# Optimization experiments

Measured on AMD Instinct MI355X. Metric: run time of the kernel, lower is better.

## Reference

```python
import jax, jax.numpy as jnp
import numpy as np

T, B, D = 4096, 128, 64
H1, H2, H3 = 20, 10, 1
L1, L2 = 20, 10


def setup_inputs() -> dict:
    key = jax.random.key(0)
    ks = iter(jax.random.split(key, 24))
    s = 0.1
    rn = lambda k, shape: (jax.random.normal(k, shape, jnp.float32) * s)
    return dict(
        x=jax.random.normal(next(ks), (T, B, D), jnp.float32),
        # stack 1: layer 0 (input D -> H1), then L1-1 layers (H1 -> H1)
        s1_wih0=rn(next(ks), (H1, D)), s1_whh0=rn(next(ks), (H1, H1)),
        s1_bih0=rn(next(ks), (H1,)), s1_bhh0=rn(next(ks), (H1,)),
        s1_wih=rn(next(ks), (L1 - 1, H1, H1)), s1_whh=rn(next(ks), (L1 - 1, H1, H1)),
        s1_bih=rn(next(ks), (L1 - 1, H1)), s1_bhh=rn(next(ks), (L1 - 1, H1)),
        # stack 2: layer 0 (H1 -> H2), then L2-1 layers (H2 -> H2)
        s2_wih0=rn(next(ks), (H2, H1)), s2_whh0=rn(next(ks), (H2, H2)),
        s2_bih0=rn(next(ks), (H2,)), s2_bhh0=rn(next(ks), (H2,)),
        s2_wih=rn(next(ks), (L2 - 1, H2, H2)), s2_whh=rn(next(ks), (L2 - 1, H2, H2)),
        s2_bih=rn(next(ks), (L2 - 1, H2)), s2_bhh=rn(next(ks), (L2 - 1, H2)),
        # output stack: single layer (H2 -> 1)
        s3_wih=rn(next(ks), (H3, H2)), s3_whh=rn(next(ks), (H3, H3)),
        s3_bih=rn(next(ks), (H3,)), s3_bhh=rn(next(ks), (H3,)),
    )


def _rnn_layer(x, wih, whh, bih, bhh):
    # x: (T, B, In). torch nn.RNN tanh cell: h_t = tanh(W_ih x_t + b_ih + W_hh h_{t-1} + b_hh)
    xw = jnp.einsum('tbi,hi->tbh', x, wih) + bih  # hoist input projection out of the scan
    h0 = jnp.zeros((x.shape[1], whh.shape[0]), x.dtype)
    def step(h, xt):
        h = jnp.tanh(xt + h @ whh.T + bhh)
        return h, h
    hT, ys = jax.lax.scan(step, h0, xw)
    return ys, hT  # (T,B,H), (B,H)


def _stack(x, wihs, whhs, bihs, bhhs):
    # scan over homogeneous layers; carry is the full sequence
    def layer(carry, p):
        wih, whh, bih, bhh = p
        y, hT = _rnn_layer(carry, wih, whh, bih, bhh)
        return y, hT
    y, hTs = jax.lax.scan(layer, x, (wihs, whhs, bihs, bhhs))
    return y, hTs


def reference(x,
              s1_wih0, s1_whh0, s1_bih0, s1_bhh0, s1_wih, s1_whh, s1_bih, s1_bhh,
              s2_wih0, s2_whh0, s2_bih0, s2_bhh0, s2_wih, s2_whh, s2_bih, s2_bhh,
              s3_wih, s3_whh, s3_bih, s3_bhh):
    y, _ = _rnn_layer(x, s1_wih0, s1_whh0, s1_bih0, s1_bhh0)
    y, _ = _stack(y, s1_wih, s1_whh, s1_bih, s1_bhh)
    y, _ = _rnn_layer(y, s2_wih0, s2_whh0, s2_bih0, s2_bhh0)
    y, _ = _stack(y, s2_wih, s2_whh, s2_bih, s2_bhh)
    y, hT = _rnn_layer(y, s3_wih, s3_whh, s3_bih, s3_bhh)
    return y, hT[None]  # out: (T,B,1), hide: (1,B,1)
```

## Files before the change

kernel.cpp:

```cpp
#include <hip/hip_runtime.h>

#define DEVI __device__ __forceinline__
typedef float f2 __attribute__((ext_vector_type(2)));
typedef unsigned u32x2 __attribute__((ext_vector_type(2)));

constexpr int T_ = 4096, B_ = 128;
constexpr int CH = 8, NCH = T_ / CH;
constexpr int NSTEP2 = 528;
constexpr int XROW = 68;

constexpr int Y1L = 2 * CH * 20;
constexpr int Y2L = 2 * CH * 12;

struct P {
  const float* x;
  const float* w1; const float* b1;
  const float* wih[31]; const float* whh[31];
  const float* bih[31]; const float* bhh[31];
  float* out;
};

DEVI float ftanh(float x) {
  float e = __builtin_amdgcn_exp2f(x * 2.8853900817779268f);
  return 1.0f - 2.0f * __builtin_amdgcn_rcpf(e + 1.0f);
}

DEVI f2 pfma(f2 a, f2 b, f2 c) { return __builtin_elementwise_fma(a, b, c); }

DEVI void acc20u(f2& a, const float* r128, const float* r64, const f2* w) {
  float4 v0 = ((const float4*)r128)[0];
  float4 v1 = ((const float4*)r128)[1];
  float2 v2 = *(const float2*)r64;
  union { float4 f; f2 h[2]; } u0, u1; u0.f = v0; u1.f = v1;
  f2 t; t.x = v2.x; t.y = v2.y;
  a = pfma(u0.h[0], w[0], a);
  a = pfma(u0.h[1], w[1], a);
  a = pfma(u1.h[0], w[2], a);
  a = pfma(u1.h[1], w[3], a);
  a = pfma(t, w[4], a);
}

DEVI void acc12u(f2& a, const float* r128, const float* r64, const f2* w) {
  float4 v0 = *(const float4*)r128;
  float2 v2 = *(const float2*)r64;
  union { float4 f; f2 h[2]; } u; u.f = v0;
  f2 t; t.x = v2.x; t.y = v2.y;
  a = pfma(u.h[0], w[0], a);
  a = pfma(u.h[1], w[1], a);
  a = pfma(t, w[2], a);
}

DEVI float dot10(const float* r, const f2* w) {
  float4 v0 = ((const float4*)r)[0];
  float4 v1 = ((const float4*)r)[1];
  float2 v2 = *(const float2*)(r + 8);
  union { float4 f; f2 h[2]; } u0, u1; u0.f = v0; u1.f = v1;
  f2 a0{0.f, 0.f}, a1{0.f, 0.f};
  a0 = pfma(u0.h[0], w[0], a0);
  a1 = pfma(u0.h[1], w[1], a1);
  a0 = pfma(u1.h[0], w[2], a0);
  a1 = pfma(u1.h[1], w[3], a1);
  f2 t; t.x = v2.x; t.y = v2.y;
  a0 = pfma(t, w[4], a0);
  f2 s = a0 + a1;
  return s.x + s.y;
}

DEVI float redsum(f2 a) {
  const float s = a.x + a.y;
  u32x2 r = __builtin_amdgcn_permlane32_swap(__float_as_uint(s),
                                             __float_as_uint(s), false, false);
  return __uint_as_float(r.x) + __uint_as_float(r.y);
}

template <int SL>
DEVI void proj_chunk(const float* xbh, float* xww, const f2* wp, float bp,
                     bool hi) {
#pragma unroll
  for (int tt = 0; tt < CH; tt++) {
    const float* xr = xbh + SL * (CH * XROW) + tt * XROW;
    f2 a; a.x = bp; a.y = 0.f;
#pragma unroll
    for (int q = 0; q < 8; q++) {
      float4 v = ((const float4*)xr)[q];
      union { float4 f; f2 h[2]; } u; u.f = v;
      a = pfma(u.h[0], wp[2 * q], a);
      a = pfma(u.h[1], wp[2 * q + 1], a);
    }
    const float s = redsum(a);
    if (!hi) xww[SL * (CH * 20) + tt * 20] = s;
  }
}

template <int SL>
DEVI void l30_chunk(const float* y29, const f2* wi30, float b30, float wh30,
                    float& h30, float*& optr, bool st) {
#pragma unroll
  for (int tt = 0; tt < CH; tt++) {
    const float d = dot10(y29 + SL * (CH * 12) + tt * 12, wi30);
    h30 = ftanh(fmaf(h30, wh30, d + b30));
    if (st) optr[tt * B_] = h30;
  }
  optr += CH * B_;
}

DEVI void stage_proj(const P& p, int b, int lane, float* xb, float* xwf,
                     const float* y29) {
  const int jj = lane & 31;
  const bool act = jj < 20;
  const bool hi = lane >= 32;
  const int j = act ? jj : 19;
  const int ko = hi ? 32 : 0;
  f2 wp[16];
#pragma unroll
  for (int k = 0; k < 16; k++) {
    wp[k].x = p.w1[j * 64 + ko + 2 * k]; wp[k].y = p.w1[j * 64 + ko + 2 * k + 1];
  }
  const float bp = hi ? 0.f : p.b1[j];
  float* xww = xwf + j;
  const float* xbh = xb + ko;

  f2 wi30[5];
#pragma unroll
  for (int k = 0; k < 5; k++) {
    wi30[k].x = p.wih[30][2 * k];
    wi30[k].y = p.wih[30][2 * k + 1];
  }
  const float b30 = p.bih[30][0] + p.bhh[30][0];
  const float wh30 = p.whh[30][0];
  float h30 = 0.f;
  float* optr = p.out + b;
  const bool st = (lane == 0);

  const int tq = lane >> 4, qq = lane & 15;
  const float* src[2]; int dst[2];
#pragma unroll
  for (int r = 0; r < 2; r++) {
    const int row = r * 4 + tq;
    src[r] = p.x + (size_t)row * (B_ * 64) + (size_t)b * 64 + qq * 4;
    dst[r] = row * XROW + qq * 4;
  }
  float4 pf[2];
#pragma unroll
  for (int r = 0; r < 2; r++) pf[r] = *(const float4*)src[r];
#pragma unroll
  for (int r = 0; r < 2; r++) *(float4*)(xb + dst[r]) = pf[r];
#pragma unroll
  for (int r = 0; r < 2; r++) src[r] += CH * B_ * 64;

  for (int s = 0; s < NSTEP2; s += 2) {
    {
      const int c = s;
      if (c < NCH) {
        const bool more = (c + 1 < NCH);
        float4 nx[2];
        if (more) {
#pragma unroll
          for (int r = 0; r < 2; r++) { nx[r] = *(const float4*)src[r]; src[r] += CH * B_ * 64; }
        }
        if (act) proj_chunk<0>(xbh, xww, wp, bp, hi);
        if (more) {
#pragma unroll
          for (int r = 0; r < 2; r++) *(float4*)(xb + CH * XROW + dst[r]) = nx[r];
        }
      }
      if ((unsigned)(s - 16) < (unsigned)NCH)
        l30_chunk<0>(y29, wi30, b30, wh30, h30, optr, st);
      __syncthreads();
    }
    {
      const int c = s + 1;
      if (c < NCH) {
        const bool more = (c + 1 < NCH);
        float4 nx[2];
        if (more) {
#pragma unroll
          for (int r = 0; r < 2; r++) { nx[r] = *(const float4*)src[r]; src[r] += CH * B_ * 64; }
        }
        if (act) proj_chunk<1>(xbh, xww, wp, bp, hi);
        if (more) {
#pragma unroll
          for (int r = 0; r < 2; r++) *(float4*)(xb + dst[r]) = nx[r];
        }
      }
      if ((unsigned)(s + 1 - 16) < (unsigned)NCH)
        l30_chunk<1>(y29, wi30, b30, wh30, h30, optr, st);
      __syncthreads();
    }
  }
  if (st) p.out[T_ * B_ + b] = h30;
}

template <int SL, bool FIRST>
DEVI void pair_chunk(const float* yin, const float* yinB,
                     const float* yArA, const float* yArB, float* yAw,
                     const float* yBrA, const float* yBrB, float* yBw,
                     const f2* wiA, const f2* whA, const f2* wiB, const f2* whB,
                     float bA, float bB, bool hi) {
  constexpr int BASE = SL * (CH * 20);
  constexpr int PV0  = (1 - SL) * (CH * 20) + (CH - 1) * 20;
  {
    f2 a; a.x = bA; a.y = 0.f;
    if constexpr (FIRST) { const float pick = yin[BASE]; if (!hi) a.x += pick; }
    else acc20u(a, yin + BASE, yinB + BASE, wiA);
    acc20u(a, yArA + PV0, yArB + PV0, whA);
    yAw[BASE] = ftanh(redsum(a));
  }
#pragma unroll
  for (int tt = 1; tt < CH; tt++) {
    const int IN  = BASE + tt * 20;
    const int INp = IN - 20;
    const int PVB = (tt == 1) ? PV0 : (INp - 20);
    f2 bb; bb.x = bB; bb.y = 0.f;
    acc20u(bb, yArA + INp, yArB + INp, wiB);
    acc20u(bb, yBrA + PVB, yBrB + PVB, whB);
    f2 a; a.x = bA; a.y = 0.f;
    if constexpr (FIRST) { const float pick = yin[IN]; if (!hi) a.x += pick; }
    else acc20u(a, yin + IN, yinB + IN, wiA);
    acc20u(a, yArA + INp, yArB + INp, whA);
    yBw[INp] = ftanh(redsum(bb));
    yAw[IN] = ftanh(redsum(a));
  }
  {
    const int IN = BASE + (CH - 1) * 20;
    f2 bb; bb.x = bB; bb.y = 0.f;
    acc20u(bb, yArA + IN, yArB + IN, wiB);
    acc20u(bb, yBrA + IN - 20, yBrB + IN - 20, whB);
    yBw[IN] = ftanh(redsum(bb));
  }
}

template <bool PH, bool FIRST>
DEVI void pair_s1(int la, int w, const P& p, int lane, float* y1f, float* xwf) {
  const int jj = lane & 31;
  const bool act = jj < 20;
  const bool hi = lane >= 32;
  const int j = act ? jj : 19;
  const int o128 = hi ? 12 : 0, o64 = hi ? 10 : 8;
  const int lb = la + 1;
  f2 whA[5], whB[5], wiB[5], wiA[FIRST ? 1 : 5];
#pragma unroll
  for (int q = 0; q < 5; q++) {
    const int tb = hi ? (q < 4 ? 12 + 2 * q : 10) : 2 * q;
    whA[q].x = p.whh[la][j * 20 + tb]; whA[q].y = p.whh[la][j * 20 + tb + 1];
    whB[q].x = p.whh[lb][j * 20 + tb]; whB[q].y = p.whh[lb][j * 20 + tb + 1];
    wiB[q].x = p.wih[lb][j * 20 + tb]; wiB[q].y = p.wih[lb][j * 20 + tb + 1];
    if constexpr (!FIRST) {
      wiA[q].x = p.wih[la][j * 20 + tb]; wiA[q].y = p.wih[la][j * 20 + tb + 1];
    }
  }
  float bA = p.bhh[la][j];
  if constexpr (!FIRST) bA += p.bih[la][j];
  float bB = p.bih[lb][j] + p.bhh[lb][j];
  if (hi) { bA = 0.f; bB = 0.f; }

  const float* yin  = FIRST ? (xwf + j) : (y1f + (la - 1) * Y1L + o128);
  const float* yinB = FIRST ? nullptr   : (y1f + (la - 1) * Y1L + o64);
  const float* yArA = y1f + la * Y1L + o128;
  const float* yArB = y1f + la * Y1L + o64;
  float*       yAw  = y1f + la * Y1L + j;
  const float* yBrA = y1f + lb * Y1L + o128;
  const float* yBrB = y1f + lb * Y1L + o64;
  float*       yBw  = y1f + lb * Y1L + j;
  if (act) { yAw[(2 * CH - 1) * 20] = 0.f; yBw[(2 * CH - 1) * 20] = 0.f; }

  for (int s = 0; s < NSTEP2; s += 2) {
    if ((unsigned)(s - w) < (unsigned)NCH && act)
      pair_chunk<PH ? 1 : 0, FIRST>(yin, yinB, yArA, yArB, yAw, yBrA, yBrB, yBw,
                                    wiA, whA, wiB, whB, bA, bB, hi);
    __syncthreads();
    if ((unsigned)(s + 1 - w) < (unsigned)NCH && act)
      pair_chunk<PH ? 0 : 1, FIRST>(yin, yinB, yArA, yArB, yAw, yBrA, yBrB, yBw,
                                    wiA, whA, wiB, whB, bA, bB, hi);
    __syncthreads();
  }
}

template <int SL, bool WIDE>
DEVI void s2pair_chunk(const float* yi0A, const float* yi0B,
                       const float* rArA, const float* rArB, float* rAw,
                       const float* rBrA, const float* rBrB, float* rBw,
                       const f2* wiA, const f2* whA, const f2* wiB, const f2* whB,
                       float bA, float bB) {
  constexpr int B1  = SL * (CH * 20);
  constexpr int B2  = SL * (CH * 12);
  constexpr int PV0 = (1 - SL) * (CH * 12) + (CH - 1) * 12;
  {
    f2 a; a.x = bA; a.y = 0.f;
    if constexpr (WIDE) acc20u(a, yi0A + B1, yi0B + B1, wiA);
    else                acc12u(a, yi0A + B2, yi0B + B2, wiA);
    acc12u(a, rArA + PV0, rArB + PV0, whA);
    rAw[B2] = ftanh(redsum(a));
  }
#pragma unroll
  for (int tt = 1; tt < CH; tt++) {
    const int IN2 = B2 + tt * 12;
    const int INp = IN2 - 12;
    const int PVB = (tt == 1) ? PV0 : (INp - 12);
    f2 bb; bb.x = bB; bb.y = 0.f;
    acc12u(bb, rArA + INp, rArB + INp, wiB);
    acc12u(bb, rBrA + PVB, rBrB + PVB, whB);
    f2 a; a.x = bA; a.y = 0.f;
    if constexpr (WIDE) { const int IN1 = B1 + tt * 20; acc20u(a, yi0A + IN1, yi0B + IN1, wiA); }
    else                acc12u(a, yi0A + IN2, yi0B + IN2, wiA);
    acc12u(a, rArA + INp, rArB + INp, whA);
    rBw[INp] = ftanh(redsum(bb));
    rAw[IN2] = ftanh(redsum(a));
  }
  {
    const int IN2 = B2 + (CH - 1) * 12;
    f2 bb; bb.x = bB; bb.y = 0.f;
    acc12u(bb, rArA + IN2, rArB + IN2, wiB);
    acc12u(bb, rBrA + IN2 - 12, rBrB + IN2 - 12, whB);
    rBw[IN2] = ftanh(redsum(bb));
  }
}

template <bool PH, bool WIDE>
DEVI void s2pair(int lA, int w, int rin, const P& p, int lane,
                 float* y1f, float* y2f) {
  const int jj = lane & 31;
  const bool act = jj < 10;
  const bool hi = lane >= 32;
  const int j = act ? jj : 9;
  const int o128w = hi ? 12 : 0, o64w = hi ? 10 : 8;
  const int o128s = hi ? 8 : 0,  o64s = hi ? 6 : 4;
  const int lB = lA + 1;
  f2 wiA[WIDE ? 5 : 3], whA[3], wiB[3], whB[3];
  if constexpr (WIDE) {
#pragma unroll
    for (int q = 0; q < 5; q++) {
      const int tb = hi ? (q < 4 ? 12 + 2 * q : 10) : 2 * q;
      wiA[q].x = p.wih[lA][j * 20 + tb];
      wiA[q].y = p.wih[lA][j * 20 + tb + 1];
    }
  } else {
#pragma unroll
    for (int q = 0; q < 3; q++) {
      const int tb = hi ? (q == 0 ? 8 : q == 1 ? 10 : 6) : 2 * q;
      wiA[q].x = tb     < 10 ? p.wih[lA][j * 10 + tb]     : 0.f;
      wiA[q].y = tb + 1 < 10 ? p.wih[lA][j * 10 + tb + 1] : 0.f;
    }
  }
#pragma unroll
  for (int q = 0; q < 3; q++) {
    const int tb = hi ? (q == 0 ? 8 : q == 1 ? 10 : 6) : 2 * q;
    whA[q].x = tb     < 10 ? p.whh[lA][j * 10 + tb]     : 0.f;
    whA[q].y = tb + 1 < 10 ? p.whh[lA][j * 10 + tb + 1] : 0.f;
    wiB[q].x = tb     < 10 ? p.wih[lB][j * 10 + tb]     : 0.f;
    wiB[q].y = tb + 1 < 10 ? p.wih[lB][j * 10 + tb + 1] : 0.f;
    whB[q].x = tb     < 10 ? p.whh[lB][j * 10 + tb]     : 0.f;
    whB[q].y = tb + 1 < 10 ? p.whh[lB][j * 10 + tb + 1] : 0.f;
  }
  const float bA = hi ? 0.f : (p.bih[lA][j] + p.bhh[lA][j]);
  const float bB = hi ? 0.f : (p.bih[lB][j] + p.bhh[lB][j]);

  const int rA = lA - 20;
  const float* yi0A = WIDE ? (y1f + 19 * Y1L + o128w) : (y2f + rin * Y2L + o128s);
  const float* yi0B = WIDE ? (y1f + 19 * Y1L + o64w)  : (y2f + rin * Y2L + o64s);
  const float* rArA = y2f + rA * Y2L + o128s;
  const float* rArB = y2f + rA * Y2L + o64s;
  float*       rAw  = y2f + rA * Y2L + j;
  const float* rBrA = y2f + (rA + 1) * Y2L + o128s;
  const float* rBrB = y2f + (rA + 1) * Y2L + o64s;
  float*       rBw  = y2f + (rA + 1) * Y2L + j;

  if constexpr (WIDE) {
    for (int q = lane; q < 10 * Y2L; q += 64) y2f[q] = 0.f;
  }

  for (int s = 0; s < NSTEP2; s += 2) {
    if ((unsigned)(s - w) < (unsigned)NCH && act)
      s2pair_chunk<PH ? 1 : 0, WIDE>(yi0A, yi0B, rArA, rArB, rAw, rBrA, rBrB, rBw,
                                     wiA, whA, wiB, whB, bA, bB);
    __syncthreads();
    if ((unsigned)(s + 1 - w) < (unsigned)NCH && act)
      s2pair_chunk<PH ? 0 : 1, WIDE>(yi0A, yi0B, rArA, rArB, rAw, rBrA, rBrB, rBw,
                                     wiA, whA, wiB, whB, bA, bB);
    __syncthreads();
  }
}

__global__ __launch_bounds__(1024, 1) void rnn_fused(P p) {
  __shared__ alignas(16) float xbuf[2 * CH * XROW];
  __shared__ alignas(16) float xw[2 * CH * 20];
  __shared__ alignas(16) float y1[20 * Y1L];
  __shared__ alignas(16) float y2[10 * Y2L];
  const int w = threadIdx.x >> 6, lane = threadIdx.x & 63, b = blockIdx.x;
  if (w == 0)       stage_proj(p, b, lane, xbuf, xw, y2 + 9 * Y2L);
  else if (w == 1)  pair_s1<true, true>(0, 1, p, lane, y1, xw);
  else if (w <= 10) {
    const int la = 2 * (w - 1);
    if (w & 1) pair_s1<true, false>(la, w, p, lane, y1, xw);
    else       pair_s1<false, false>(la, w, p, lane, y1, xw);
  }
  else if (w == 11) s2pair<true,  true >(20, 11, 0, p, lane, y1, y2);
  else if (w == 12) s2pair<false, false>(22, 12, 1, p, lane, y1, y2);
  else if (w == 13) s2pair<true,  false>(24, 13, 3, p, lane, y1, y2);
  else if (w == 14) s2pair<false, false>(26, 14, 5, p, lane, y1, y2);
  else              s2pair<true,  false>(28, 15, 7, p, lane, y1, y2);
}

extern "C" void kernel_launch(void* const* d_in, const int* in_sizes, int n_in,
                              void* d_out, int out_size, void* d_ws, size_t ws_size,
                              hipStream_t stream) {
  (void)in_sizes; (void)out_size; (void)d_ws; (void)ws_size;
  if (n_in < 21) return;
  P p{};
  p.x  = (const float*)d_in[0];
  p.w1 = (const float*)d_in[1];
  p.b1 = (const float*)d_in[3];
  p.wih[0] = nullptr;              p.whh[0] = (const float*)d_in[2];
  p.bih[0] = nullptr;              p.bhh[0] = (const float*)d_in[4];
  for (int l = 1; l < 20; l++) {
    p.wih[l] = (const float*)d_in[5] + (l - 1) * 400;
    p.whh[l] = (const float*)d_in[6] + (l - 1) * 400;
    p.bih[l] = (const float*)d_in[7] + (l - 1) * 20;
    p.bhh[l] = (const float*)d_in[8] + (l - 1) * 20;
  }
  p.wih[20] = (const float*)d_in[9];   p.whh[20] = (const float*)d_in[10];
  p.bih[20] = (const float*)d_in[11];  p.bhh[20] = (const float*)d_in[12];
  for (int l = 21; l < 30; l++) {
    p.wih[l] = (const float*)d_in[13] + (l - 21) * 100;
    p.whh[l] = (const float*)d_in[14] + (l - 21) * 100;
    p.bih[l] = (const float*)d_in[15] + (l - 21) * 10;
    p.bhh[l] = (const float*)d_in[16] + (l - 21) * 10;
  }
  p.wih[30] = (const float*)d_in[17];  p.whh[30] = (const float*)d_in[18];
  p.bih[30] = (const float*)d_in[19];  p.bhh[30] = (const float*)d_in[20];
  p.out = (float*)d_out;

  rnn_fused<<<B_, 1024, 0, stream>>>(p);
}
```

Baseline: 1.607 ms.

## Split each batch's layer pipeline across two workgroups linked by a global ring

Each batch element's wavefront pipeline is now split across two 576-thread workgroups instead of one 1024-thread workgroup. The first block runs the input projection and layers 0-13. The second runs layers 14-30. Layer-13 output passes between them through a 16-chunk ring buffer in workspace memory, with producer and consumer counters held as agent-scope atomics and spin-wait sleeps. The aim is to spread the 31-layer wavefront over twice as many CUs and shorten per-block barrier chains. The cost is global-memory handoff latency, spin-waiting, and a reliance on both blocks of a pair being resident at the same time.

```diff
diff --git a/kernel.cpp b/kernel.cpp
--- a/kernel.cpp
+++ b/kernel.cpp
@@ -11,6 +11,10 @@
 
 constexpr int Y1L = 2 * CH * 20;
 constexpr int Y2L = 2 * CH * 12;
+
+constexpr int RQ = 16;
+constexpr int NSF = NCH + 8;
+constexpr int NSB = NCH + 20;
 
 struct P {
   const float* x;
@@ -191,12 +195,70 @@
   if (st) p.out[T_ * B_ + b] = h30;
 }
 
-template <int SL, bool FIRST>
+DEVI void stage_proj_f(const P& p, int b, int lane, float* xb, float* xwf,
+                       int nstep) {
+  const int jj = lane & 31;
+  const bool act = jj < 20;
+  const bool hi = lane >= 32;
+  const int j = act ? jj : 19;
+  const int ko = hi ? 32 : 0;
+  f2 wp[16];
+#pragma unroll
+  for (int k = 0; k < 16; k++) {
+    wp[k].x = p.w1[j * 64 + ko + 2 * k]; wp[k].y = p.w1[j * 64 + ko + 2 * k + 1];
+  }
+  const float bp = hi ? 0.f : p.b1[j];
+  float* xww = xwf + j;
+  const float* xbh = xb + ko;
+
+  const int tq = lane >> 4, qq = lane & 15;
+  const float* src[2]; int dst[2];
+#pragma unroll
+  for (int r = 0; r < 2; r++) {
+    const int row = r * 4 + tq;
+    src[r] = p.x + (size_t)row * (B_ * 64) + (size_t)b * 64 + qq * 4;
+    dst[r] = row * XROW + qq * 4;
+  }
+  float4 pf[2];
+#pragma unroll
+  for (int r = 0; r < 2; r++) pf[r] = *(const float4*)src[r];
+#pragma unroll
+  for (int r = 0; r < 2; r++) *(float4*)(xb + dst[r]) = pf[r];
+#pragma unroll
+  for (int r = 0; r < 2; r++) src[r] += CH * B_ * 64;
+
+  for (int s = 0; s < nstep; s += 2) {
+#pragma unroll
+    for (int ph = 0; ph < 2; ph++) {
+      const int c = s + ph;
+      if (c < NCH) {
+        const bool more = (c + 1 < NCH);
+        float4 nx[2];
+        if (more) {
+#pragma unroll
+          for (int r = 0; r < 2; r++) { nx[r] = *(const float4*)src[r]; src[r] += CH * B_ * 64; }
+        }
+        if (act) {
+          if (c & 1) proj_chunk<1>(xbh, xww, wp, bp, hi);
+          else       proj_chunk<0>(xbh, xww, wp, bp, hi);
+        }
+        if (more) {
+          const int sl = ((c + 1) & 1) * (CH * XROW);
+#pragma unroll
+          for (int r = 0; r < 2; r++) *(float4*)(xb + sl + dst[r]) = nx[r];
+        }
+      }
+      __syncthreads();
+    }
+  }
+}
+
+template <int SL, bool FIRST, bool PROD = false>
 DEVI void pair_chunk(const float* yin, const float* yinB,
                      const float* yArA, const float* yArB, float* yAw,
                      const float* yBrA, const float* yBrB, float* yBw,
                      const f2* wiA, const f2* whA, const f2* wiB, const f2* whB,
-                     float bA, float bB, bool hi) {
+                     float bA, float bB, bool hi, float* gw = nullptr) {
   constexpr int BASE = SL * (CH * 20);
   constexpr int PV0  = (1 - SL) * (CH * 20) + (CH - 1) * 20;
   {
@@ -218,7 +280,9 @@
     if constexpr (FIRST) { const float pick = yin[IN]; if (!hi) a.x += pick; }
     else acc20u(a, yin + IN, yinB + IN, wiA);
     acc20u(a, yArA + INp, yArB + INp, whA);
-    yBw[INp] = ftanh(redsum(bb));
+    const float hb = ftanh(redsum(bb));
+    yBw[INp] = hb;
+    if constexpr (PROD) { if (!hi) gw[(tt - 1) * 20] = hb; }
     yAw[IN] = ftanh(redsum(a));
   }
   {
@@ -226,7 +290,9 @@
     f2 bb; bb.x = bB; bb.y = 0.f;
     acc20u(bb, yArA + IN, yArB + IN, wiB);
     acc20u(bb, yBrA + IN - 20, yBrB + IN - 20, whB);
-    yBw[IN] = ftanh(redsum(bb));
+    const float hb = ftanh(redsum(bb));
+    yBw[IN] = hb;
+    if constexpr (PROD) { if (!hi) gw[(CH - 1) * 20] = hb; }
   }
 }
 
@@ -273,6 +339,71 @@
       pair_chunk<PH ? 0 : 1, FIRST>(yin, yinB, yArA, yArB, yAw, yBrA, yBrB, yBw,
                                     wiA, whA, wiB, whB, bA, bB, hi);
     __syncthreads();
+  }
+}
+
+template <bool FIRST, bool PROD>
+DEVI void pair_drv(int la, int w, int nstep, const P& p, int lane,
+                   const float* xwf, const float* rIn, float* rA, float* rB,
+                   float* gring, unsigned* prog, unsigned* cons) {
+  const int jj = lane & 31;
+  const bool act = jj < 20;
+  const bool hi = lane >= 32;
+  const int j = act ? jj : 19;
+  const int o128 = hi ? 12 : 0, o64 = hi ? 10 : 8;
+  const int lb = la + 1;
+  f2 whA[5], whB[5], wiB[5], wiA[FIRST ? 1 : 5];
+#pragma unroll
+  for (int q = 0; q < 5; q++) {
+    const int tb = hi ? (q < 4 ? 12 + 2 * q : 10) : 2 * q;
+    whA[q].x = p.whh[la][j * 20 + tb]; whA[q].y = p.whh[la][j * 20 + tb + 1];
+    whB[q].x = p.whh[lb][j * 20 + tb]; whB[q].y = p.whh[lb][j * 20 + tb + 1];
+    wiB[q].x = p.wih[lb][j * 20 + tb]; wiB[q].y = p.wih[lb][j * 20 + tb + 1];
+    if constexpr (!FIRST) {
+      wiA[q].x = p.wih[la][j * 20 + tb]; wiA[q].y = p.wih[la][j * 20 + tb + 1];
+    }
+  }
+  float bA = p.bhh[la][j];
+  if constexpr (!FIRST) bA += p.bih[la][j];
+  float bB = p.bih[lb][j] + p.bhh[lb][j];
+  if (hi) { bA = 0.f; bB = 0.f; }
+
+  const float* yin  = FIRST ? (xwf + j) : (rIn + o128);
+  const float* yinB = FIRST ? nullptr   : (rIn + o64);
+  const float* yArA = rA + o128; const float* yArB = rA + o64;
+  float* yAw = rA + j;
+  const float* yBrA = rB + o128; const float* yBrB = rB + o64;
+  float* yBw = rB + j;
+  if (act) { yAw[(2 * CH - 1) * 20] = 0.f; yBw[(2 * CH - 1) * 20] = 0.f; }
+
+  for (int s = 0; s < nstep; s += 2) {
+#pragma unroll
+    for (int ph = 0; ph < 2; ph++) {
+      const int c = s + ph - w;
+      if ((unsigned)c < (unsigned)NCH && act) {
+        float* gw = nullptr;
+        if constexpr (PROD) {
+          if (c >= RQ) {
+            while ((int)c - (int)__hip_atomic_load(cons, __ATOMIC_RELAXED,
+                     __HIP_MEMORY_SCOPE_AGENT) >= RQ)
+              __builtin_amdgcn_s_sleep(8);
+          }
+          gw = gring + (c & (RQ - 1)) * (CH * 20) + j;
+        }
+        if (c & 1)
+          pair_chunk<1, FIRST, PROD>(yin, yinB, yArA, yArB, yAw, yBrA, yBrB,
+                                     yBw, wiA, whA, wiB, whB, bA, bB, hi, gw);
+        else
+          pair_chunk<0, FIRST, PROD>(yin, yinB, yArA, yArB, yAw, yBrA, yBrB,
+                                     yBw, wiA, whA, wiB, whB, bA, bB, hi, gw);
+        if constexpr (PROD) {
+          if (lane == 0)
+            __hip_atomic_store(prog, (unsigned)(c + 1), __ATOMIC_RELEASE,
+                               __HIP_MEMORY_SCOPE_AGENT);
+        }
+      }
+      __syncthreads();
+    }
   }
 }
 
@@ -381,6 +512,119 @@
   }
 }
 
+template <bool WIDE>
+DEVI void s2_drv(int lA, int w, int nstep, const P& p, int lane,
+                 const float* wideRow, const float* rinRow, float* y2f) {
+  const int jj = lane & 31;
+  const bool act = jj < 10;
+  const bool hi = lane >= 32;
+  const int j = act ? jj : 9;
+  const int o128w = hi ? 12 : 0, o64w = hi ? 10 : 8;
+  const int o128s = hi ? 8 : 0,  o64s = hi ? 6 : 4;
+  const int lB = lA + 1;
+  f2 wiA[WIDE ? 5 : 3], whA[3], wiB[3], whB[3];
+  if constexpr (WIDE) {
+#pragma unroll
+    for (int q = 0; q < 5; q++) {
+      const int tb = hi ? (q < 4 ? 12 + 2 * q : 10) : 2 * q;
+      wiA[q].x = p.wih[lA][j * 20 + tb];
+      wiA[q].y = p.wih[lA][j * 20 + tb + 1];
+    }
+  } else {
+#pragma unroll
+    for (int q = 0; q < 3; q++) {
+      const int tb = hi ? (q == 0 ? 8 : q == 1 ? 10 : 6) : 2 * q;
+      wiA[q].x = tb     < 10 ? p.wih[lA][j * 10 + tb]     : 0.f;
+      wiA[q].y = tb + 1 < 10 ? p.wih[lA][j * 10 + tb + 1] : 0.f;
+    }
+  }
+#pragma unroll
+  for (int q = 0; q < 3; q++) {
+    const int tb = hi ? (q == 0 ? 8 : q == 1 ? 10 : 6) : 2 * q;
+    whA[q].x = tb     < 10 ? p.whh[lA][j * 10 + tb]     : 0.f;
+    whA[q].y = tb + 1 < 10 ? p.whh[lA][j * 10 + tb + 1] : 0.f;
+    wiB[q].x = tb     < 10 ? p.wih[lB][j * 10 + tb]     : 0.f;
+    wiB[q].y = tb + 1 < 10 ? p.wih[lB][j * 10 + tb + 1] : 0.f;
+    whB[q].x = tb     < 10 ? p.whh[lB][j * 10 + tb]     : 0.f;
+    whB[q].y = tb + 1 < 10 ? p.whh[lB][j * 10 + tb + 1] : 0.f;
+  }
+  const float bA = hi ? 0.f : (p.bih[lA][j] + p.bhh[lA][j]);
+  const float bB = hi ? 0.f : (p.bih[lB][j] + p.bhh[lB][j]);
+
+  const int rA = lA - 20;
+  const float* yi0A = WIDE ? (wideRow + o128w) : (rinRow + o128s);
+  const float* yi0B = WIDE ? (wideRow + o64w)  : (rinRow + o64s);
+  const float* rArA = y2f + rA * Y2L + o128s;
+  const float* rArB = y2f + rA * Y2L + o64s;
+  float*       rAw  = y2f + rA * Y2L + j;
+  const float* rBrA = y2f + (rA + 1) * Y2L + o128s;
+  const float* rBrB = y2f + (rA + 1) * Y2L + o64s;
+  float*       rBw  = y2f + (rA + 1) * Y2L + j;
+
+  if constexpr (WIDE) {
+    for (int q = lane; q < 10 * Y2L; q += 64) y2f[q] = 0.f;
+  }
+
+  for (int s = 0; s < nstep; s += 2) {
+#pragma unroll
+    for (int ph = 0; ph < 2; ph++) {
+      const int c = s + ph - w;
+      if ((unsigned)c < (unsigned)NCH && act) {
+        if (c & 1)
+          s2pair_chunk<1, WIDE>(yi0A, yi0B, rArA, rArB, rAw, rBrA, rBrB, rBw,
+                                wiA, whA, wiB, whB, bA, bB);
+        else
+          s2pair_chunk<0, WIDE>(yi0A, yi0B, rArA, rArB, rAw, rBrA, rBrB, rBw,
+                                wiA, whA, wiB, whB, bA, bB);
+      }
+      __syncthreads();
+    }
+  }
+}
+
+DEVI void stager_l30(const P& p, int b, int lane, float* row0, const float* y29,
+                     const float* gring, unsigned* prog, unsigned* cons,
+                     int nstep) {
+  f2 wi30[5];
+#pragma unroll
+  for (int k = 0; k < 5; k++) {
+    wi30[k].x = p.wih[30][2 * k];
+    wi30[k].y = p.wih[30][2 * k + 1];
+  }
+  const float b30 = p.bih[30][0] + p.bhh[30][0];
+  const float wh30 = p.whh[30][0];
+  float h30 = 0.f;
+  float* optr = p.out + b;
+  const bool st = (lane == 0);
+
+  for (int s = 0; s < nstep; s += 2) {
+#pragma unroll
+    for (int ph = 0; ph < 2; ph++) {
+      const int sp = s + ph;
+      const int cs = sp - 9;
+      if ((unsigned)cs < (unsigned)NCH) {
+        while ((int)__hip_atomic_load(prog, __ATOMIC_ACQUIRE,
+                 __HIP_MEMORY_SCOPE_AGENT) < cs + 1)
+          __builtin_amdgcn_s_sleep(8);
+        if (lane < 40) {
+          const float4 v = *(const float4*)(gring + (cs & (RQ - 1)) * (CH * 20) + lane * 4);
+          *(float4*)(row0 + (cs & 1) * (CH * 20) + lane * 4) = v;
+        }
+        if (lane == 0)
+          __hip_atomic_store(cons, (unsigned)(cs + 1), __ATOMIC_RELAXED,
+                             __HIP_MEMORY_SCOPE_AGENT);
+      }
+      const int cl = sp - 18;
+      if ((unsigned)cl < (unsigned)NCH) {
+        if (cl & 1) l30_chunk<1>(y29, wi30, b30, wh30, h30, optr, st);
+        else        l30_chunk<0>(y29, wi30, b30, wh30, h30, optr, st);
+      }
+      __syncthreads();
+    }
+  }
+  if (st) p.out[T_ * B_ + b] = h30;
+}
+
 __global__ __launch_bounds__(1024, 1) void rnn_fused(P p) {
   __shared__ alignas(16) float xbuf[2 * CH * XROW];
   __shared__ alignas(16) float xw[2 * CH * 20];
@@ -401,10 +645,67 @@
   else              s2pair<true,  false>(28, 15, 7, p, lane, y1, y2);
 }
 
+__global__ void rnn_init(unsigned* f) {
+  if (threadIdx.x < 2 * B_) f[threadIdx.x] = 0;
+}
+
+__global__ __launch_bounds__(576) void rnn_split(P p, float* ring, unsigned* flags) {
+  __shared__ alignas(16) float lds[21000];
+  const int w = threadIdx.x >> 6, lane = threadIdx.x & 63;
+  const int b = blockIdx.x >> 1, role = blockIdx.x & 1;
+  float* gring = ring + (size_t)b * (RQ * CH * 20);
+  unsigned* prog = flags + b;
+  unsigned* cons = flags + B_ + b;
+
+  if (role == 0) {
+    float* xbuf = lds;
+    float* xw   = lds + 1088;
+    float* y1f  = lds + 1408;
+    if (w == 0) {
+      stage_proj_f(p, b, lane, xbuf, xw, NSF);
+    } else if (w == 1) {
+      pair_drv<true, false>(0, 1, NSF, p, lane, xw, nullptr,
+                            y1f, y1f + Y1L, nullptr, nullptr, nullptr);
+    } else if (w <= 6) {
+      const int la = 2 * (w - 1);
+      pair_drv<false, false>(la, w, NSF, p, lane, nullptr,
+                             y1f + (la - 1) * Y1L, y1f + la * Y1L,
+                             y1f + (la + 1) * Y1L, nullptr, nullptr, nullptr);
+    } else if (w == 7) {
+      pair_drv<false, true>(12, 7, NSF, p, lane, nullptr,
+                            y1f + 11 * Y1L, y1f + 12 * Y1L, y1f + 13 * Y1L,
+                            gring, prog, cons);
+    } else {
+      for (int s = 0; s < NSF; s += 2) { __syncthreads(); __syncthreads(); }
+    }
+  } else {
+    float* y1b = lds;
+    float* y2  = lds + 2240;
+    if (w == 0) {
+      pair_drv<false, false>(14, 10, NSB, p, lane, nullptr,
+                             y1b, y1b + Y1L, y1b + 2 * Y1L, nullptr, nullptr, nullptr);
+    } else if (w == 1) {
+      pair_drv<false, false>(16, 11, NSB, p, lane, nullptr,
+                             y1b + 2 * Y1L, y1b + 3 * Y1L, y1b + 4 * Y1L,
+                             nullptr, nullptr, nullptr);
+    } else if (w == 2) {
+      pair_drv<false, false>(18, 12, NSB, p, lane, nullptr,
+                             y1b + 4 * Y1L, y1b + 5 * Y1L, y1b + 6 * Y1L,
+                             nullptr, nullptr, nullptr);
+    }
+    else if (w == 3) s2_drv<true >(20, 13, NSB, p, lane, y1b + 6 * Y1L, nullptr, y2);
+    else if (w == 4) s2_drv<false>(22, 14, NSB, p, lane, nullptr, y2 + 1 * Y2L, y2);
+    else if (w == 5) s2_drv<false>(24, 15, NSB, p, lane, nullptr, y2 + 3 * Y2L, y2);
+    else if (w == 6) s2_drv<false>(26, 16, NSB, p, lane, nullptr, y2 + 5 * Y2L, y2);
+    else if (w == 7) s2_drv<false>(28, 17, NSB, p, lane, nullptr, y2 + 7 * Y2L, y2);
+    else stager_l30(p, b, lane, y1b, y2 + 9 * Y2L, gring, prog, cons, NSB);
+  }
+}
+
 extern "C" void kernel_launch(void* const* d_in, const int* in_sizes, int n_in,
                               void* d_out, int out_size, void* d_ws, size_t ws_size,
                               hipStream_t stream) {
-  (void)in_sizes; (void)out_size; (void)d_ws; (void)ws_size;
+  (void)in_sizes; (void)out_size;
   if (n_in < 21) return;
   P p{};
   p.x  = (const float*)d_in[0];
@@ -430,5 +731,14 @@
   p.bih[30] = (const float*)d_in[19];  p.bhh[30] = (const float*)d_in[20];
   p.out = (float*)d_out;
 
-  rnn_fused<<<B_, 1024, 0, stream>>>(p);
-}
+  const size_t ringBytes = (size_t)B_ * RQ * CH * 20 * sizeof(float);
+  const size_t need = ringBytes + 2 * B_ * sizeof(unsigned);
+  if (d_ws != nullptr && ws_size >= need) {
+    float* ring = (float*)d_ws;
+    unsigned* flags = (unsigned*)((char*)d_ws + ringBytes);
+    rnn_init<<<1, 256, 0, stream>>>(flags);
+    rnn_split<<<2 * B_, 576, 0, stream>>>(p, ring, flags);
+  } else {
+    rnn_fused<<<B_, 1024, 0, stream>>>(p);
+  }
+}
```

Measured after the change: 3.882 ms. 141% more time.
